# Optimization experiments

Hardware: AMD Instinct MI355X
Metric: run time of the kernel (lower is better)

Reference implementation:

```python
import jax, jax.numpy as jnp
import numpy as np

N_NODES = 250000
N_EDGES = 5000000


def setup_inputs() -> dict:
    key = jax.random.key(0)
    k1, k2, k3, k4, k5, k6 = jax.random.split(key, 6)
    x = jax.random.normal(k1, (N_NODES, 1), dtype=jnp.float32)
    edge_index = jax.random.randint(k2, (2, N_EDGES), 0, N_NODES, dtype=jnp.int64)
    # Glorot-style small weights like PyG GCNConv init
    W1 = jax.random.normal(k3, (1, 16), dtype=jnp.float32) * (1.0 / np.sqrt(1 + 16))
    b1 = jnp.zeros((16,), dtype=jnp.float32)
    W2 = jax.random.normal(k4, (16, 2), dtype=jnp.float32) * (1.0 / np.sqrt(16 + 2))
    b2 = jnp.zeros((2,), dtype=jnp.float32)
    return {"x": x, "edge_index": edge_index, "W1": W1, "b1": b1, "W2": W2, "b2": b2}


def _gcn_conv(x, row, col, W, b, n_nodes):
    """PyG GCNConv: x' = D^{-1/2} (A + I) D^{-1/2} (x W) + b.

    row = source nodes, col = target nodes (messages flow row -> col).
    Self-loops are assumed already appended to row/col.
    """
    h = x @ W  # [N, out]
    ones = jnp.ones(row.shape[0], dtype=h.dtype)
    deg = jax.ops.segment_sum(ones, col, num_segments=n_nodes)  # in-degree incl. self-loop
    dinv = jnp.where(deg > 0, jax.lax.rsqrt(deg), 0.0)
    norm = dinv[row] * dinv[col]  # [E+N]
    msg = h[row] * norm[:, None]  # gather + scale  [E+N, out]
    out = jax.ops.segment_sum(msg, col, num_segments=n_nodes)  # scatter-add
    return out + b


def reference(x, edge_index, W1, b1, W2, b2):
    n = x.shape[0]
    loop = jnp.arange(n, dtype=edge_index.dtype)
    row = jnp.concatenate([edge_index[0], loop])
    col = jnp.concatenate([edge_index[1], loop])
    h = _gcn_conv(x, row, col, W1, b1, n)
    h = jax.nn.relu(h)
    # F.dropout(training=False) at inference -> identity
    h = _gcn_conv(h, row, col, W2, b2, n)
    return jax.nn.softmax(h, axis=1)
```

## Files before the change

kernel.cpp:

```cpp
#include <hip/hip_runtime.h>

#define ST 512
#define PT 20
#define EPB (ST * PT)
#define CSHIFT 10
#define CMASK 1023u
#define CW 1024
#define NCMAX 255
#define CAP 24576


__global__ void k_init(unsigned* __restrict__ gcur, int NC) {
    for (int b = threadIdx.x; b < NC; b += blockDim.x)
        gcur[b] = (unsigned)b * CAP;
}

__global__ __launch_bounds__(ST) void k_sortk(const int* __restrict__ row,
                                              const int* __restrict__ col,
                                              unsigned* __restrict__ gcur,
                                              unsigned* __restrict__ pack1,
                                              int E, int NC) {
    __shared__ unsigned loff[NCMAX + 2];
    __shared__ unsigned gbase[NCMAX + 1];
    __shared__ unsigned cur[NCMAX + 1];
    __shared__ unsigned staging[EPB];

    const int t = threadIdx.x;
    for (int i = t; i <= NC; i += ST) loff[i] = 0;
    __syncthreads();

    const int base = blockIdx.x * EPB;
    int c[PT];

#pragma unroll
    for (int k = 0; k < PT / 4; ++k) {
        int e = base + (k * ST + t) * 4;
        int4 cc;
        if (e + 3 < E) {
            cc = *reinterpret_cast<const int4*>(col + e);
        } else {
            cc.x = (e     < E) ? col[e]     : -1;
            cc.y = (e + 1 < E) ? col[e + 1] : -1;
            cc.z = (e + 2 < E) ? col[e + 2] : -1;
            cc.w = (e + 3 < E) ? col[e + 3] : -1;
        }
        c[4 * k] = cc.x; c[4 * k + 1] = cc.y; c[4 * k + 2] = cc.z; c[4 * k + 3] = cc.w;
    }
#pragma unroll
    for (int k = 0; k < PT; ++k)
        if (c[k] >= 0) atomicAdd(&loff[((unsigned)c[k] >> CSHIFT) + 1], 1u);
    __syncthreads();

    if (t < 64) {
        unsigned v[4];
        unsigned ls = 0;
#pragma unroll
        for (int k = 0; k < 4; ++k) {
            int idx = t * 4 + k;
            v[k] = (idx <= NC) ? loff[idx] : 0;
            ls += v[k];
        }
        unsigned sc = ls;
#pragma unroll
        for (int d = 1; d < 64; d <<= 1) {
            unsigned n = __shfl_up(sc, d, 64);
            if (t >= d) sc += n;
        }
        unsigned run = sc - ls;
#pragma unroll
        for (int k = 0; k < 4; ++k) {
            int idx = t * 4 + k;
            run += v[k];
            if (idx <= NC) loff[idx] = run;
        }
    }
    __syncthreads();

    if (t < NC) {
        unsigned cb = loff[t + 1] - loff[t];
        gbase[t] = atomicAdd(&gcur[t], cb);
        cur[t] = loff[t];
    }
    __syncthreads();

#pragma unroll
    for (int k = 0; k < PT / 4; ++k) {
        int e = base + (k * ST + t) * 4;
        int4 rr = make_int4(0, 0, 0, 0);
        if (e + 3 < E) {
            rr = *reinterpret_cast<const int4*>(row + e);
        } else {
            rr.x = (e     < E) ? row[e]     : 0;
            rr.y = (e + 1 < E) ? row[e + 1] : 0;
            rr.z = (e + 2 < E) ? row[e + 2] : 0;
            rr.w = (e + 3 < E) ? row[e + 3] : 0;
        }
        int rl[4] = {rr.x, rr.y, rr.z, rr.w};
#pragma unroll
        for (int j = 0; j < 4; ++j) {
            int cc = c[4 * k + j];
            if (cc >= 0) {
                unsigned b = (unsigned)cc >> CSHIFT;
                unsigned p = atomicAdd(&cur[b], 1u);
                staging[p] = ((unsigned)rl[j] << CSHIFT) | ((unsigned)cc & CMASK);
            }
        }
    }
    __syncthreads();

    const int wave = t >> 6;
    const int lane = t & 63;
    for (int b = wave; b < NC; b += ST / 64) {
        unsigned lo = loff[b];
        unsigned hi = loff[b + 1];
        unsigned gb = gbase[b];
        unsigned lim = (unsigned)(b + 1) * CAP;
        for (unsigned i = lo + lane; i < hi; i += 64) {
            unsigned pos = gb + (i - lo);
            if (pos < lim)
                pack1[pos] = staging[i];
        }
    }
}


__global__ __launch_bounds__(CW) void k_degk(const unsigned* __restrict__ pack1,
                                             const unsigned* __restrict__ gcur,
                                             const float* __restrict__ x,
                                             float* __restrict__ dinv, float* __restrict__ xs,
                                             int N) {
    __shared__ unsigned dcnt[CW];
    const int b = blockIdx.x;
    const int t = threadIdx.x;
    dcnt[t] = 0;
    __syncthreads();
    unsigned s0 = (unsigned)b * CAP;
    unsigned s1 = min(gcur[b], s0 + (unsigned)CAP);
    unsigned n4 = (s1 - s0) >> 2;
    for (unsigned i = t; i < n4; i += CW) {
        uint4 p = reinterpret_cast<const uint4*>(pack1 + s0)[i];
        atomicAdd(&dcnt[p.x & CMASK], 1u);
        atomicAdd(&dcnt[p.y & CMASK], 1u);
        atomicAdd(&dcnt[p.z & CMASK], 1u);
        atomicAdd(&dcnt[p.w & CMASK], 1u);
    }
    unsigned i = s0 + (n4 << 2) + t;
    if (i < s1) atomicAdd(&dcnt[pack1[i] & CMASK], 1u);
    __syncthreads();
    int v = (b << CSHIFT) + t;
    if (v < N) {
        float di = rsqrtf((float)dcnt[t] + 1.0f);
        dinv[v] = di;
        xs[v] = di * x[v];
    }
}

__global__ __launch_bounds__(CW) void k_l1k(const unsigned* __restrict__ pack1,
                                            const unsigned* __restrict__ gcur,
                                            const float* __restrict__ xs,
                                            const float* __restrict__ dinv,
                                            const float* __restrict__ W1,
                                            const float* __restrict__ b1,
                                            const float* __restrict__ W2,
                                            float* __restrict__ gs, int N) {
    __shared__ float acc[CW];
    const int b = blockIdx.x;
    const int t = threadIdx.x;
    acc[t] = 0.0f;
    __syncthreads();
    unsigned s0 = (unsigned)b * CAP;
    unsigned s1 = min(gcur[b], s0 + (unsigned)CAP);
    unsigned n4 = (s1 - s0) >> 2;
    const uint4* pk = reinterpret_cast<const uint4*>(pack1 + s0);
    unsigned i = t;
    for (; i + CW < n4; i += 2 * CW) {
        uint4 pa = pk[i];
        uint4 pb = pk[i + CW];
        float a0 = xs[pa.x >> CSHIFT];
        float a1 = xs[pa.y >> CSHIFT];
        float a2 = xs[pa.z >> CSHIFT];
        float a3 = xs[pa.w >> CSHIFT];
        float c0 = xs[pb.x >> CSHIFT];
        float c1 = xs[pb.y >> CSHIFT];
        float c2 = xs[pb.z >> CSHIFT];
        float c3 = xs[pb.w >> CSHIFT];
        atomicAdd(&acc[pa.x & CMASK], a0);
        atomicAdd(&acc[pa.y & CMASK], a1);
        atomicAdd(&acc[pa.z & CMASK], a2);
        atomicAdd(&acc[pa.w & CMASK], a3);
        atomicAdd(&acc[pb.x & CMASK], c0);
        atomicAdd(&acc[pb.y & CMASK], c1);
        atomicAdd(&acc[pb.z & CMASK], c2);
        atomicAdd(&acc[pb.w & CMASK], c3);
    }
    if (i < n4) {
        uint4 pa = pk[i];
        float a0 = xs[pa.x >> CSHIFT];
        float a1 = xs[pa.y >> CSHIFT];
        float a2 = xs[pa.z >> CSHIFT];
        float a3 = xs[pa.w >> CSHIFT];
        atomicAdd(&acc[pa.x & CMASK], a0);
        atomicAdd(&acc[pa.y & CMASK], a1);
        atomicAdd(&acc[pa.z & CMASK], a2);
        atomicAdd(&acc[pa.w & CMASK], a3);
    }
    unsigned j = s0 + (n4 << 2) + t;
    if (j < s1) {
        unsigned p = pack1[j];
        atomicAdd(&acc[p & CMASK], xs[p >> CSHIFT]);
    }
    __syncthreads();
    int v = (b << CSHIFT) + t;
    if (v < N) {
        float di = dinv[v];
        float tt = di * (acc[t] + xs[v]);
        float g = 0.0f;
#pragma unroll
        for (int jj = 0; jj < 16; ++jj) {
            float y = fmaxf(fmaf(W1[jj], tt, b1[jj]), 0.0f);
            g = fmaf(W2[2 * jj] - W2[2 * jj + 1], y, g);
        }
        gs[v] = di * g;
    }
}

__global__ __launch_bounds__(CW) void k_l2k(const unsigned* __restrict__ pack1,
                                            const unsigned* __restrict__ gcur,
                                            const float* __restrict__ gs,
                                            const float* __restrict__ dinv,
                                            const float* __restrict__ b2,
                                            float* __restrict__ out, int N) {
    __shared__ float acc[CW];
    const int b = blockIdx.x;
    const int t = threadIdx.x;
    acc[t] = 0.0f;
    __syncthreads();
    unsigned s0 = (unsigned)b * CAP;
    unsigned s1 = min(gcur[b], s0 + (unsigned)CAP);
    unsigned n4 = (s1 - s0) >> 2;
    const uint4* pk = reinterpret_cast<const uint4*>(pack1 + s0);
    unsigned i = t;
    for (; i + CW < n4; i += 2 * CW) {
        uint4 pa = pk[i];
        uint4 pb = pk[i + CW];
        float a0 = gs[pa.x >> CSHIFT];
        float a1 = gs[pa.y >> CSHIFT];
        float a2 = gs[pa.z >> CSHIFT];
        float a3 = gs[pa.w >> CSHIFT];
        float c0 = gs[pb.x >> CSHIFT];
        float c1 = gs[pb.y >> CSHIFT];
        float c2 = gs[pb.z >> CSHIFT];
        float c3 = gs[pb.w >> CSHIFT];
        atomicAdd(&acc[pa.x & CMASK], a0);
        atomicAdd(&acc[pa.y & CMASK], a1);
        atomicAdd(&acc[pa.z & CMASK], a2);
        atomicAdd(&acc[pa.w & CMASK], a3);
        atomicAdd(&acc[pb.x & CMASK], c0);
        atomicAdd(&acc[pb.y & CMASK], c1);
        atomicAdd(&acc[pb.z & CMASK], c2);
        atomicAdd(&acc[pb.w & CMASK], c3);
    }
    if (i < n4) {
        uint4 pa = pk[i];
        float a0 = gs[pa.x >> CSHIFT];
        float a1 = gs[pa.y >> CSHIFT];
        float a2 = gs[pa.z >> CSHIFT];
        float a3 = gs[pa.w >> CSHIFT];
        atomicAdd(&acc[pa.x & CMASK], a0);
        atomicAdd(&acc[pa.y & CMASK], a1);
        atomicAdd(&acc[pa.z & CMASK], a2);
        atomicAdd(&acc[pa.w & CMASK], a3);
    }
    unsigned j = s0 + (n4 << 2) + t;
    if (j < s1) {
        unsigned p = pack1[j];
        atomicAdd(&acc[p & CMASK], gs[p >> CSHIFT]);
    }
    __syncthreads();
    int v = (b << CSHIFT) + t;
    if (v < N) {
        float diff = dinv[v] * (acc[t] + gs[v]) + (b2[0] - b2[1]);
        float p0 = 1.0f / (1.0f + __expf(-diff));
        float2 o;
        o.x = p0;
        o.y = 1.0f - p0;
        reinterpret_cast<float2*>(out)[v] = o;
    }
}

__global__ void k_zero_f(float* __restrict__ p, int n) {
    int i = blockIdx.x * blockDim.x + threadIdx.x;
    int v = i * 4;
    if (v + 3 < n) {
        reinterpret_cast<float4*>(p + v)[0] = make_float4(0.f, 0.f, 0.f, 0.f);
    } else {
        for (; v < n; ++v) p[v] = 0.0f;
    }
}
__global__ void k_deg_f(const int* __restrict__ col, float* __restrict__ deg, int E) {
    int i = blockIdx.x * blockDim.x + threadIdx.x;
    int e = i * 4;
    if (e + 3 < E) {
        int4 c = reinterpret_cast<const int4*>(col + e)[0];
        atomicAdd(deg + c.x, 1.0f); atomicAdd(deg + c.y, 1.0f);
        atomicAdd(deg + c.z, 1.0f); atomicAdd(deg + c.w, 1.0f);
    } else {
        for (; e < E; ++e) atomicAdd(deg + col[e], 1.0f);
    }
}
__global__ void k_node1_f(const float* __restrict__ x, float* __restrict__ degdinv,
                          float* __restrict__ xs, int N) {
    int v = blockIdx.x * blockDim.x + threadIdx.x;
    if (v < N) {
        float dinv = rsqrtf(degdinv[v] + 1.0f);
        degdinv[v] = dinv;
        xs[v] = dinv * x[v];
    }
}
__global__ void k_scat_f(const int* __restrict__ row, const int* __restrict__ col,
                         const float* __restrict__ src, float* __restrict__ acc, int E) {
    int i = blockIdx.x * blockDim.x + threadIdx.x;
    int e = i * 4;
    if (e + 3 < E) {
        int4 r = reinterpret_cast<const int4*>(row + e)[0];
        int4 c = reinterpret_cast<const int4*>(col + e)[0];
        float s0 = src[r.x], s1 = src[r.y], s2 = src[r.z], s3 = src[r.w];
        atomicAdd(acc + c.x, s0); atomicAdd(acc + c.y, s1);
        atomicAdd(acc + c.z, s2); atomicAdd(acc + c.w, s3);
    } else {
        for (; e < E; ++e) atomicAdd(acc + col[e], src[row[e]]);
    }
}
__global__ void k_mlp_f(const float* __restrict__ W1, const float* __restrict__ b1,
                        const float* __restrict__ W2, const float* __restrict__ dinv,
                        float* __restrict__ acc, float* __restrict__ xsgs, int N) {
    int v = blockIdx.x * blockDim.x + threadIdx.x;
    if (v < N) {
        float di = dinv[v];
        float t = di * (acc[v] + xsgs[v]);
        float g = 0.0f;
#pragma unroll
        for (int j = 0; j < 16; ++j) {
            float y = fmaxf(fmaf(W1[j], t, b1[j]), 0.0f);
            g = fmaf(W2[2 * j] - W2[2 * j + 1], y, g);
        }
        xsgs[v] = di * g;
        acc[v] = 0.0f;
    }
}
__global__ void k_out_f(const float* __restrict__ b2, const float* __restrict__ dinv,
                        const float* __restrict__ acc, const float* __restrict__ gs,
                        float* __restrict__ out, int N) {
    int v = blockIdx.x * blockDim.x + threadIdx.x;
    if (v < N) {
        float diff = dinv[v] * (acc[v] + gs[v]) + (b2[0] - b2[1]);
        float p0 = 1.0f / (1.0f + __expf(-diff));
        float2 o; o.x = p0; o.y = 1.0f - p0;
        reinterpret_cast<float2*>(out)[v] = o;
    }
}

extern "C" void kernel_launch(void* const* d_in, const int* in_sizes, int n_in,
                              void* d_out, int out_size, void* d_ws, size_t ws_size,
                              hipStream_t stream) {
    const float* x  = (const float*)d_in[0];
    const int* edge = (const int*)d_in[1];
    const float* W1 = (const float*)d_in[2];
    const float* b1 = (const float*)d_in[3];
    const float* W2 = (const float*)d_in[4];
    const float* b2 = (const float*)d_in[5];
    float* out = (float*)d_out;

    const int N = in_sizes[0];
    const int E = in_sizes[1] / 2;
    const int* row = edge;
    const int* col = edge + E;

    const int NC  = (N + CW - 1) >> CSHIFT;
    const int NBS = (E + EPB - 1) / EPB;

    const double mean = (double)E / NC;
    const double slack = mean + 8.0 * __builtin_sqrt(mean > 1.0 ? mean : 1.0);
    const size_t need = ((size_t)NC * CAP + NC) * 4 + (size_t)3 * N * 4;

    if (NC <= NCMAX && N < (1 << 22) && slack < CAP && ws_size >= need) {
        unsigned* pack1 = (unsigned*)d_ws;
        unsigned* gcur  = pack1 + (size_t)NC * CAP;
        float* dinv     = (float*)(gcur + NC);
        float* xs       = dinv + N;
        float* gs       = xs + N;

        k_init <<<1, 256, 0, stream>>>(gcur, NC);
        k_sortk<<<NBS, ST, 0, stream>>>(row, col, gcur, pack1, E, NC);
        k_degk <<<NC, CW, 0, stream>>>(pack1, gcur, x, dinv, xs, N);
        k_l1k  <<<NC, CW, 0, stream>>>(pack1, gcur, xs, dinv, W1, b1, W2, gs, N);
        k_l2k  <<<NC, CW, 0, stream>>>(pack1, gcur, gs, dinv, b2, out, N);
    } else {
        float* w0 = (float*)d_ws;
        float* w1 = w0 + N;
        float* w2 = w1 + N;
        const int nb = (N + 255) / 256;
        const int eb = ((E + 3) / 4 + 255) / 256;
        const int zb = ((2 * N + 3) / 4 + 255) / 256;
        k_zero_f <<<zb, 256, 0, stream>>>(w0, 2 * N);
        k_deg_f  <<<eb, 256, 0, stream>>>(col, w0, E);
        k_node1_f<<<nb, 256, 0, stream>>>(x, w0, w2, N);
        k_scat_f <<<eb, 256, 0, stream>>>(row, col, w2, w1, E);
        k_mlp_f  <<<nb, 256, 0, stream>>>(W1, b1, W2, w0, w1, w2, N);
        k_scat_f <<<eb, 256, 0, stream>>>(row, col, w2, w1, E);
        k_out_f  <<<nb, 256, 0, stream>>>(b2, w0, w1, w2, out, N);
    }
}
```

Measured before the change: 174.4 us.

## Fuse degree counting into sort kernel via global atomics and drop degree pass

Counts in-degrees with global atomics on a per-node array inside the bucketing sort kernel. This replaces the separate kernel that re-read the packed edge buckets to count degrees in shared memory. A small vectorized node kernel then computes dinv and the scaled features. The init kernel is replaced by a memset, and bucket cursors become relative counts. The change saves a full pass over the packed edges, but adds millions of scattered global atomics to the sort kernel.

```diff
diff --git a/kernel.cpp b/kernel.cpp
--- a/kernel.cpp
+++ b/kernel.cpp
@@ -10,14 +10,10 @@
 #define CAP 24576
 
 
-__global__ void k_init(unsigned* __restrict__ gcur, int NC) {
-    for (int b = threadIdx.x; b < NC; b += blockDim.x)
-        gcur[b] = (unsigned)b * CAP;
-}
-
 __global__ __launch_bounds__(ST) void k_sortk(const int* __restrict__ row,
                                               const int* __restrict__ col,
                                               unsigned* __restrict__ gcur,
+                                              unsigned* __restrict__ deg,
                                               unsigned* __restrict__ pack1,
                                               int E, int NC) {
     __shared__ unsigned loff[NCMAX + 2];
@@ -46,6 +42,11 @@
         }
         c[4 * k] = cc.x; c[4 * k + 1] = cc.y; c[4 * k + 2] = cc.z; c[4 * k + 3] = cc.w;
     }
+
+#pragma unroll
+    for (int k = 0; k < PT; ++k)
+        if (c[k] >= 0) atomicAdd(&deg[c[k]], 1u);
+
 #pragma unroll
     for (int k = 0; k < PT; ++k)
         if (c[k] >= 0) atomicAdd(&loff[((unsigned)c[k] >> CSHIFT) + 1], 1u);
@@ -114,46 +115,40 @@
         unsigned lo = loff[b];
         unsigned hi = loff[b + 1];
         unsigned gb = gbase[b];
-        unsigned lim = (unsigned)(b + 1) * CAP;
         for (unsigned i = lo + lane; i < hi; i += 64) {
-            unsigned pos = gb + (i - lo);
-            if (pos < lim)
-                pack1[pos] = staging[i];
-        }
-    }
-}
-
-
-__global__ __launch_bounds__(CW) void k_degk(const unsigned* __restrict__ pack1,
-                                             const unsigned* __restrict__ gcur,
-                                             const float* __restrict__ x,
-                                             float* __restrict__ dinv, float* __restrict__ xs,
-                                             int N) {
-    __shared__ unsigned dcnt[CW];
-    const int b = blockIdx.x;
-    const int t = threadIdx.x;
-    dcnt[t] = 0;
-    __syncthreads();
-    unsigned s0 = (unsigned)b * CAP;
-    unsigned s1 = min(gcur[b], s0 + (unsigned)CAP);
-    unsigned n4 = (s1 - s0) >> 2;
-    for (unsigned i = t; i < n4; i += CW) {
-        uint4 p = reinterpret_cast<const uint4*>(pack1 + s0)[i];
-        atomicAdd(&dcnt[p.x & CMASK], 1u);
-        atomicAdd(&dcnt[p.y & CMASK], 1u);
-        atomicAdd(&dcnt[p.z & CMASK], 1u);
-        atomicAdd(&dcnt[p.w & CMASK], 1u);
-    }
-    unsigned i = s0 + (n4 << 2) + t;
-    if (i < s1) atomicAdd(&dcnt[pack1[i] & CMASK], 1u);
-    __syncthreads();
-    int v = (b << CSHIFT) + t;
-    if (v < N) {
-        float di = rsqrtf((float)dcnt[t] + 1.0f);
-        dinv[v] = di;
-        xs[v] = di * x[v];
-    }
-}
+            unsigned off = gb + (i - lo);
+            if (off < CAP)
+                pack1[(unsigned)b * CAP + off] = staging[i];
+        }
+    }
+}
+
+
+__global__ __launch_bounds__(256) void k_nodek(const unsigned* __restrict__ deg,
+                                               const float* __restrict__ x,
+                                               float* __restrict__ dinv,
+                                               float* __restrict__ xs, int N) {
+    int i = blockIdx.x * blockDim.x + threadIdx.x;
+    int v = i * 4;
+    if (v + 3 < N) {
+        uint4 d = *reinterpret_cast<const uint4*>(deg + v);
+        float4 xx = *reinterpret_cast<const float4*>(x + v);
+        float4 di, xv;
+        di.x = rsqrtf((float)d.x + 1.0f); xv.x = di.x * xx.x;
+        di.y = rsqrtf((float)d.y + 1.0f); xv.y = di.y * xx.y;
+        di.z = rsqrtf((float)d.z + 1.0f); xv.z = di.z * xx.z;
+        di.w = rsqrtf((float)d.w + 1.0f); xv.w = di.w * xx.w;
+        *reinterpret_cast<float4*>(dinv + v) = di;
+        *reinterpret_cast<float4*>(xs + v) = xv;
+    } else {
+        for (; v < N; ++v) {
+            float di = rsqrtf((float)deg[v] + 1.0f);
+            dinv[v] = di;
+            xs[v] = di * x[v];
+        }
+    }
+}
+
 
 __global__ __launch_bounds__(CW) void k_l1k(const unsigned* __restrict__ pack1,
                                             const unsigned* __restrict__ gcur,
@@ -168,9 +163,11 @@
     const int t = threadIdx.x;
     acc[t] = 0.0f;
     __syncthreads();
+    unsigned cnt = gcur[b];
+    if (cnt > CAP) cnt = CAP;
     unsigned s0 = (unsigned)b * CAP;
-    unsigned s1 = min(gcur[b], s0 + (unsigned)CAP);
-    unsigned n4 = (s1 - s0) >> 2;
+    unsigned s1 = s0 + cnt;
+    unsigned n4 = cnt >> 2;
     const uint4* pk = reinterpret_cast<const uint4*>(pack1 + s0);
     unsigned i = t;
     for (; i + CW < n4; i += 2 * CW) {
@@ -235,9 +232,11 @@
     const int t = threadIdx.x;
     acc[t] = 0.0f;
     __syncthreads();
+    unsigned cnt = gcur[b];
+    if (cnt > CAP) cnt = CAP;
     unsigned s0 = (unsigned)b * CAP;
-    unsigned s1 = min(gcur[b], s0 + (unsigned)CAP);
-    unsigned n4 = (s1 - s0) >> 2;
+    unsigned s1 = s0 + cnt;
+    unsigned n4 = cnt >> 2;
     const uint4* pk = reinterpret_cast<const uint4*>(pack1 + s0);
     unsigned i = t;
     for (; i + CW < n4; i += 2 * CW) {
@@ -381,18 +380,21 @@
 
     const double mean = (double)E / NC;
     const double slack = mean + 8.0 * __builtin_sqrt(mean > 1.0 ? mean : 1.0);
-    const size_t need = ((size_t)NC * CAP + NC) * 4 + (size_t)3 * N * 4;
+    const size_t need = ((size_t)NC * CAP + NC + (size_t)4 * N) * 4;
 
     if (NC <= NCMAX && N < (1 << 22) && slack < CAP && ws_size >= need) {
         unsigned* pack1 = (unsigned*)d_ws;
         unsigned* gcur  = pack1 + (size_t)NC * CAP;
-        float* dinv     = (float*)(gcur + NC);
+        unsigned* deg   = gcur + NC;
+        float* dinv     = (float*)(deg + N);
         float* xs       = dinv + N;
         float* gs       = xs + N;
 
-        k_init <<<1, 256, 0, stream>>>(gcur, NC);
-        k_sortk<<<NBS, ST, 0, stream>>>(row, col, gcur, pack1, E, NC);
-        k_degk <<<NC, CW, 0, stream>>>(pack1, gcur, x, dinv, xs, N);
+        const int nb4 = ((N + 3) / 4 + 255) / 256;
+
+        hipMemsetAsync(gcur, 0, (size_t)(NC + N) * sizeof(unsigned), stream);
+        k_sortk<<<NBS, ST, 0, stream>>>(row, col, gcur, deg, pack1, E, NC);
+        k_nodek<<<nb4, 256, 0, stream>>>(deg, x, dinv, xs, N);
         k_l1k  <<<NC, CW, 0, stream>>>(pack1, gcur, xs, dinv, W1, b1, W2, gs, N);
         k_l2k  <<<NC, CW, 0, stream>>>(pack1, gcur, gs, dinv, b2, out, N);
     } else {
```

Measured after the change: 355.2 us. 2.04x slower.
